# Kernel tuning notes

Measured on AMD Instinct MI355X. Metric: run time of the kernel, lower is better.

The kernel has to match this reference:

```python
import jax, jax.numpy as jnp
import numpy as np

N_NODES = 50000
N_EDGES = 800000
D = 96
H2 = 32
OUT = 4


def _glorot(key, shape):
    fan_in, fan_out = shape[0], shape[1]
    lim = (6.0 / (fan_in + fan_out)) ** 0.5
    return jax.random.uniform(key, shape, jnp.float32, -lim, lim)


def setup_inputs() -> dict:
    key = jax.random.key(0)
    ks = jax.random.split(key, 12)
    x = jax.random.normal(ks[0], (N_NODES, D), jnp.float32)
    edge_index = jax.random.randint(ks[1], (2, N_EDGES), 0, N_NODES, jnp.int32)
    return {
        "x": x,
        "edge_index": edge_index,
        "eps1": jnp.float32(0.0),
        "eps2": jnp.float32(0.0),
        "W1a": _glorot(ks[2], (D, D)),  "b1a": jnp.zeros((D,), jnp.float32),
        "W1b": _glorot(ks[3], (D, D)),  "b1b": jnp.zeros((D,), jnp.float32),
        "W2a": _glorot(ks[4], (D, H2)), "b2a": jnp.zeros((H2,), jnp.float32),
        "W2b": _glorot(ks[5], (H2, H2)),"b2b": jnp.zeros((H2,), jnp.float32),
        "Wh": _glorot(ks[6], (H2, OUT)),"bh": jnp.zeros((OUT,), jnp.float32),
    }


def _gin_agg(h, src, dst):
    # sum_{j in N(i)} h_j : gather source features, scatter-add to destination
    return jax.ops.segment_sum(h[src], dst, num_segments=N_NODES)


def reference(x, edge_index, eps1, eps2, W1a, b1a, W1b, b1b, W2a, b2a, W2b, b2b, Wh, bh):
    src, dst = edge_index[0], edge_index[1]

    # GIN layer 1: mlp1((1+eps1)*x + agg(x)), then outer ReLU (dropout is eval-mode identity)
    z = (1.0 + eps1) * x + _gin_agg(x, src, dst)           # [N, D]
    h = jax.nn.relu(z @ W1a + b1a) @ W1b + b1b             # mlp1
    h = jax.nn.relu(h)

    # GIN layer 2: mlp2((1+eps2)*h + agg(h)), then outer ReLU
    z2 = (1.0 + eps2) * h + _gin_agg(h, src, dst)          # [N, D]
    h2 = jax.nn.relu(z2 @ W2a + b2a) @ W2b + b2b           # mlp2 -> [N, 32]
    h2 = jax.nn.relu(h2)

    return h2 @ Wh + bh                                    # [N, 4]
```

## Files before the change

### kernel.cpp

```cpp
#include <hip/hip_runtime.h>

#define NN 50000
#define NE 800000
#define DD 96
#define HH 32
#define OO 4
#define ELLW 64
#define NBUCK 196
#define BCAP 8192

typedef unsigned short ushort_t;
typedef unsigned int uint_t;
typedef __attribute__((ext_vector_type(8))) short short8;
typedef __attribute__((ext_vector_type(4))) float f32x4;

__device__ inline ushort_t f2bf(float f) {
    uint_t b = __float_as_uint(f);
    return (ushort_t)((b + 0x7fffu + ((b >> 16) & 1u)) >> 16);
}

__device__ inline void addbf8(float* a, uint4 u) {
    a[0] += __uint_as_float(u.x << 16);
    a[1] += __uint_as_float(u.x & 0xffff0000u);
    a[2] += __uint_as_float(u.y << 16);
    a[3] += __uint_as_float(u.y & 0xffff0000u);
    a[4] += __uint_as_float(u.z << 16);
    a[5] += __uint_as_float(u.z & 0xffff0000u);
    a[6] += __uint_as_float(u.w << 16);
    a[7] += __uint_as_float(u.w & 0xffff0000u);
}


#define BA_B   98
#define WF_B   6
#define MT1    (NN / 16)
#define MFMA1_B ((MT1 + 3) / 4)

__global__ void k_big1(const int* __restrict__ edges, int* __restrict__ bcnt,
                       uint_t* __restrict__ packed,
                       const float* __restrict__ W1b, const float* __restrict__ W2a,
                       ushort_t* __restrict__ wf,
                       const float* __restrict__ x, const float* __restrict__ W1a,
                       ushort_t* __restrict__ y1) {
    int b = blockIdx.x;
    if (b < BA_B) {
        __shared__ int hist[NBUCK];
        __shared__ int basesh[NBUCK];
        int thr = threadIdx.x;
        if (thr < NBUCK) hist[thr] = 0;
        __syncthreads();
#pragma unroll
        for (int k = 0; k < 8; ++k) {
            int t4 = b * 2048 + k * 256 + thr;
            if (t4 < NE / 4) {
                int4 tt = ((const int4*)(edges + NE))[t4];
                atomicAdd(&hist[tt.x >> 8], 1);
                atomicAdd(&hist[tt.y >> 8], 1);
                atomicAdd(&hist[tt.z >> 8], 1);
                atomicAdd(&hist[tt.w >> 8], 1);
            }
        }
        __syncthreads();
        if (thr < NBUCK) {
            int c = hist[thr];
            basesh[thr] = c ? atomicAdd(&bcnt[thr], c) : 0;
        }
        __syncthreads();
        if (thr < NBUCK) hist[thr] = 0;
        __syncthreads();
#pragma unroll
        for (int k = 0; k < 8; ++k) {
            int t4 = b * 2048 + k * 256 + thr;
            if (t4 < NE / 4) {
                int4 ss = ((const int4*)edges)[t4];
                int4 tt = ((const int4*)(edges + NE))[t4];
                int b0 = tt.x >> 8, b1 = tt.y >> 8, b2 = tt.z >> 8, b3 = tt.w >> 8;
                int p0 = basesh[b0] + atomicAdd(&hist[b0], 1);
                int p1 = basesh[b1] + atomicAdd(&hist[b1], 1);
                int p2 = basesh[b2] + atomicAdd(&hist[b2], 1);
                int p3 = basesh[b3] + atomicAdd(&hist[b3], 1);
                if (p0 < BCAP) packed[(size_t)b0 * BCAP + p0] = ((uint_t)ss.x << 8) | (tt.x & 255);
                if (p1 < BCAP) packed[(size_t)b1 * BCAP + p1] = ((uint_t)ss.y << 8) | (tt.y & 255);
                if (p2 < BCAP) packed[(size_t)b2 * BCAP + p2] = ((uint_t)ss.z << 8) | (tt.z & 255);
                if (p3 < BCAP) packed[(size_t)b3 * BCAP + p3] = ((uint_t)ss.w << 8) | (tt.w & 255);
            }
        }
        return;
    }
    b -= BA_B;
    if (b < WF_B) {
        int tw = b * 256 + threadIdx.x;
        if (tw < 1152 + 384) {
            const float* Wsrc; ushort_t* dst; int KOUT, fl;
            if (tw < 1152) { Wsrc = W1b; dst = wf;        KOUT = DD; fl = tw; }
            else           { Wsrc = W2a; dst = wf + 9216; KOUT = HH; fl = tw - 1152; }
            int lane = fl & 63;
            int fc = fl >> 6;
            int c = fc % 3, nt = fc / 3;
            int kb = c * 32 + (lane >> 4) * 8;
            int col = nt * 16 + (lane & 15);
            ushort_t v[8];
#pragma unroll
            for (int j = 0; j < 8; ++j)
                v[j] = f2bf(Wsrc[(size_t)(kb + j) * KOUT + col]);
            *(uint4*)(dst + (size_t)fl * 8) = *(uint4*)v;
        }
        return;
    }
    b -= WF_B;
    constexpr int KC = 3, NT = 6;
    int lane = threadIdx.x & 63;
    int widx = threadIdx.x >> 6;
    int tile = b * 4 + widx;
    if (tile >= MT1) return;
    int row0 = tile * 16;
    int q = lane >> 4;
    int l16 = lane & 15;

    short8 bf[NT][KC];
#pragma unroll
    for (int nt = 0; nt < NT; ++nt)
#pragma unroll
        for (int c = 0; c < KC; ++c) {
            ushort_t v[8];
#pragma unroll
            for (int j = 0; j < 8; ++j)
                v[j] = f2bf(W1a[(size_t)(c * 32 + q * 8 + j) * DD + nt * 16 + l16]);
            bf[nt][c] = *(short8*)v;
        }

    short8 af[KC];
#pragma unroll
    for (int c = 0; c < KC; ++c) {
        const float* ap = x + (size_t)(row0 + l16) * DD + c * 32 + q * 8;
        float4 f0 = *(const float4*)ap;
        float4 f1 = *(const float4*)(ap + 4);
        ushort_t v[8] = {f2bf(f0.x), f2bf(f0.y), f2bf(f0.z), f2bf(f0.w),
                         f2bf(f1.x), f2bf(f1.y), f2bf(f1.z), f2bf(f1.w)};
        af[c] = *(short8*)v;
    }

    f32x4 acc[NT];
#pragma unroll
    for (int nt = 0; nt < NT; ++nt) acc[nt] = (f32x4){0.f, 0.f, 0.f, 0.f};
#pragma unroll
    for (int nt = 0; nt < NT; ++nt)
#pragma unroll
        for (int c = 0; c < KC; ++c)
            acc[nt] = __builtin_amdgcn_mfma_f32_16x16x32_bf16(af[c], bf[nt][c], acc[nt], 0, 0, 0);

#pragma unroll
    for (int nt = 0; nt < NT; ++nt) {
        int s = nt >> 1;
        int c32 = (nt & 1) * 16 + l16;
#pragma unroll
        for (int r = 0; r < 4; ++r)
            y1[(size_t)s * NN * 32 + (size_t)(row0 + q * 4 + r) * 32 + c32] = f2bf(acc[nt][r]);
    }
}


__global__ void k_bucketB(const int* __restrict__ bcnt, const uint_t* __restrict__ packed,
                          ushort_t* __restrict__ ell, int* __restrict__ deg) {
    __shared__ int curL[256];
    int b = blockIdx.x;
    int thr = threadIdx.x;
    int n0 = b * 256;
    curL[thr] = 0;
    __syncthreads();
    int cnt = min(bcnt[b], BCAP);
    const uint_t* pk = packed + (size_t)b * BCAP;
    for (int e = thr; e < cnt; e += 256) {
        uint_t u = pk[e];
        int doff = u & 255;
        int src = u >> 8;
        int p = atomicAdd(&curL[doff], 1);
        if (p < ELLW) ell[(size_t)(n0 + doff) * ELLW + p] = (ushort_t)src;
    }
    __syncthreads();
    if (n0 + thr < NN) deg[n0 + thr] = curL[thr];
}


__global__ void k_aggb96(const ushort_t* __restrict__ y, const int* __restrict__ deg,
                         const ushort_t* __restrict__ ell, const float* __restrict__ eps_p,
                         const float* __restrict__ b, ushort_t* __restrict__ out) {
    int idx = blockIdx.x * blockDim.x + threadIdx.x;
    if (idx >= NN * 24) return;
    int s = idx / (NN * 8);
    int rem = idx - s * (NN * 8);
    int i = rem >> 3;
    int sub = rem & 7;
    int v = sub >> 1, part = sub & 1;
    const uint4* ys = (const uint4*)(y + (size_t)s * NN * 32);
    const ushort_t* er = ell + (size_t)i * ELLW;
    int d = min(deg[i], ELLW);
    float a0[8] = {0,0,0,0,0,0,0,0}, a1[8] = {0,0,0,0,0,0,0,0};
    float a2[8] = {0,0,0,0,0,0,0,0}, a3[8] = {0,0,0,0,0,0,0,0};
    int p = part;
    for (; p + 6 < d; p += 8) {
        int s0 = er[p], s1 = er[p+2], s2 = er[p+4], s3 = er[p+6];
        uint4 f0 = ys[(size_t)s0 * 4 + v];
        uint4 f1 = ys[(size_t)s1 * 4 + v];
        uint4 f2 = ys[(size_t)s2 * 4 + v];
        uint4 f3 = ys[(size_t)s3 * 4 + v];
        addbf8(a0, f0); addbf8(a1, f1); addbf8(a2, f2); addbf8(a3, f3);
    }
    for (; p < d; p += 2) addbf8(a0, ys[(size_t)er[p] * 4 + v]);

    float sm[8];
#pragma unroll
    for (int k = 0; k < 8; ++k) {
        sm[k] = (a0[k] + a1[k]) + (a2[k] + a3[k]);
        sm[k] += __shfl_xor(sm[k], 1);
    }
    if (part) return;

    uint4 su = ys[(size_t)i * 4 + v];
    float s8[8];
    s8[0] = __uint_as_float(su.x << 16); s8[1] = __uint_as_float(su.x & 0xffff0000u);
    s8[2] = __uint_as_float(su.y << 16); s8[3] = __uint_as_float(su.y & 0xffff0000u);
    s8[4] = __uint_as_float(su.z << 16); s8[5] = __uint_as_float(su.z & 0xffff0000u);
    s8[6] = __uint_as_float(su.w << 16); s8[7] = __uint_as_float(su.w & 0xffff0000u);
    float4 bl = ((const float4*)b)[s * 8 + v * 2];
    float4 bhv = ((const float4*)b)[s * 8 + v * 2 + 1];
    float bb[8] = {bl.x, bl.y, bl.z, bl.w, bhv.x, bhv.y, bhv.z, bhv.w};
    float e = 1.0f + eps_p[0];
    ushort_t r[8];
#pragma unroll
    for (int k = 0; k < 8; ++k) {
        float vv = fmaf(e, s8[k], sm[k]) + bb[k];
        r[k] = f2bf(fmaxf(vv, 0.0f));
    }
    uint4 o;
    o.x = (uint_t)r[0] | ((uint_t)r[1] << 16);
    o.y = (uint_t)r[2] | ((uint_t)r[3] << 16);
    o.z = (uint_t)r[4] | ((uint_t)r[5] << 16);
    o.w = (uint_t)r[6] | ((uint_t)r[7] << 16);
    ((uint4*)out)[(size_t)i * 12 + s * 4 + v] = o;
}


#define HSTRIDE 104

__global__ void k_mfma23(const ushort_t* __restrict__ t1, const ushort_t* __restrict__ wf,
                         const float* __restrict__ b1b, ushort_t* __restrict__ y2) {
    constexpr int KC = 3, NT1 = 6, NT2 = 2;
    __shared__ __align__(16) ushort_t hT[4][16 * HSTRIDE];
    int lane = threadIdx.x & 63;
    int widx = threadIdx.x >> 6;
    int tile = blockIdx.x * 4 + widx;
    bool live = tile < MT1;
    int row0 = tile * 16;
    int q = lane >> 4;
    int l16 = lane & 15;
    const short8* bfp1 = (const short8*)wf;
    const short8* bfp2 = (const short8*)(wf + 9216);

    if (live) {
        short8 bf[NT1][KC];
#pragma unroll
        for (int nt = 0; nt < NT1; ++nt)
#pragma unroll
            for (int c = 0; c < KC; ++c)
                bf[nt][c] = bfp1[(nt * KC + c) * 64 + lane];

        short8 af[KC];
#pragma unroll
        for (int c = 0; c < KC; ++c) {
            uint4 av = *(const uint4*)(t1 + (size_t)(row0 + l16) * DD + c * 32 + q * 8);
            af[c] = *(short8*)&av;
        }

        f32x4 acc[NT1];
#pragma unroll
        for (int nt = 0; nt < NT1; ++nt) acc[nt] = (f32x4){0.f, 0.f, 0.f, 0.f};
#pragma unroll
        for (int nt = 0; nt < NT1; ++nt)
#pragma unroll
            for (int c = 0; c < KC; ++c)
                acc[nt] = __builtin_amdgcn_mfma_f32_16x16x32_bf16(af[c], bf[nt][c], acc[nt], 0, 0, 0);

#pragma unroll
        for (int nt = 0; nt < NT1; ++nt) {
            int col = nt * 16 + l16;
            float bv = b1b[col];
#pragma unroll
            for (int r = 0; r < 4; ++r)
                hT[widx][(q * 4 + r) * HSTRIDE + col] = f2bf(fmaxf(acc[nt][r] + bv, 0.0f));
        }
    }
    __syncthreads();
    if (!live) return;

    short8 af2[KC];
#pragma unroll
    for (int c = 0; c < KC; ++c) {
        uint4 av = *(const uint4*)&hT[widx][l16 * HSTRIDE + c * 32 + q * 8];
        af2[c] = *(short8*)&av;
    }
    short8 bf2[NT2][KC];
#pragma unroll
    for (int nt = 0; nt < NT2; ++nt)
#pragma unroll
        for (int c = 0; c < KC; ++c)
            bf2[nt][c] = bfp2[(nt * KC + c) * 64 + lane];

    f32x4 acc2[NT2];
#pragma unroll
    for (int nt = 0; nt < NT2; ++nt) acc2[nt] = (f32x4){0.f, 0.f, 0.f, 0.f};
#pragma unroll
    for (int nt = 0; nt < NT2; ++nt)
#pragma unroll
        for (int c = 0; c < KC; ++c)
            acc2[nt] = __builtin_amdgcn_mfma_f32_16x16x32_bf16(af2[c], bf2[nt][c], acc2[nt], 0, 0, 0);

#pragma unroll
    for (int nt = 0; nt < NT2; ++nt) {
        int col = nt * 16 + l16;
#pragma unroll
        for (int r = 0; r < 4; ++r)
            y2[(size_t)(row0 + q * 4 + r) * HH + col] = f2bf(acc2[nt][r]);
    }
}


#define TSTRIDE 36
#define ATR 16

__global__ void k_aggtail(const ushort_t* __restrict__ y2, const int* __restrict__ deg,
                          const ushort_t* __restrict__ ell, const float* __restrict__ eps_p,
                          const float* __restrict__ b2a, const float* __restrict__ W2b,
                          const float* __restrict__ b2b, const float* __restrict__ Wh,
                          const float* __restrict__ bhp, float* __restrict__ out) {
    __shared__ float t2f[ATR * TSTRIDE];
    int row = threadIdx.x >> 4;
    int sub = threadIdx.x & 15;
    int jg = sub & 3;
    int part = sub >> 2;
    int i = blockIdx.x * ATR + row;
    bool live = i < NN;

    if (live) {
        const uint4* y4 = (const uint4*)y2;
        const ushort_t* er = ell + (size_t)i * ELLW;
        int d = min(deg[i], ELLW);
        float a0[8] = {0,0,0,0,0,0,0,0}, a1[8] = {0,0,0,0,0,0,0,0};
        int p = part;
        for (; p + 4 < d; p += 8) {
            int s0 = er[p], s1 = er[p + 4];
            uint4 f0 = y4[(size_t)s0 * 4 + jg];
            uint4 f1 = y4[(size_t)s1 * 4 + jg];
            addbf8(a0, f0); addbf8(a1, f1);
        }
        for (; p < d; p += 4) addbf8(a0, y4[(size_t)er[p] * 4 + jg]);

        float s[8];
#pragma unroll
        for (int k = 0; k < 8; ++k) {
            s[k] = a0[k] + a1[k];
            s[k] += __shfl_xor(s[k], 4);
            s[k] += __shfl_xor(s[k], 8);
        }
        if (part == 0) {
            uint4 su = y4[(size_t)i * 4 + jg];
            float s8[8];
            s8[0] = __uint_as_float(su.x << 16); s8[1] = __uint_as_float(su.x & 0xffff0000u);
            s8[2] = __uint_as_float(su.y << 16); s8[3] = __uint_as_float(su.y & 0xffff0000u);
            s8[4] = __uint_as_float(su.z << 16); s8[5] = __uint_as_float(su.z & 0xffff0000u);
            s8[6] = __uint_as_float(su.w << 16); s8[7] = __uint_as_float(su.w & 0xffff0000u);
            float4 bl = ((const float4*)b2a)[2 * jg];
            float4 bhv = ((const float4*)b2a)[2 * jg + 1];
            float bb[8] = {bl.x, bl.y, bl.z, bl.w, bhv.x, bhv.y, bhv.z, bhv.w};
            float e = 1.0f + eps_p[0];
#pragma unroll
            for (int k = 0; k < 8; ++k) {
                float vv = fmaf(e, s8[k], s[k]) + bb[k];
                t2f[row * TSTRIDE + jg * 8 + k] = fmaxf(vv, 0.0f);
            }
        }
    }
    __syncthreads();

    float o[OO] = {0.f, 0.f, 0.f, 0.f};
    if (live) {
        const float* tr = &t2f[row * TSTRIDE];
#pragma unroll
        for (int jj = 0; jj < 2; ++jj) {
            int j = sub * 2 + jj;
            float acc = b2b[j];
#pragma unroll 8
            for (int k = 0; k < HH; ++k)
                acc = fmaf(tr[k], W2b[k * HH + j], acc);
            acc = fmaxf(acc, 0.0f);
#pragma unroll
            for (int oo = 0; oo < OO; ++oo)
                o[oo] = fmaf(acc, Wh[j * OO + oo], o[oo]);
        }
    }
#pragma unroll
    for (int oo = 0; oo < OO; ++oo) {
        o[oo] += __shfl_xor(o[oo], 1);
        o[oo] += __shfl_xor(o[oo], 2);
        o[oo] += __shfl_xor(o[oo], 4);
        o[oo] += __shfl_xor(o[oo], 8);
    }
    if (live && sub == 0) {
        float4 ov = {o[0] + bhp[0], o[1] + bhp[1], o[2] + bhp[2], o[3] + bhp[3]};
        ((float4*)out)[i] = ov;
    }
}


extern "C" void kernel_launch(void* const* d_in, const int* in_sizes, int n_in,
                              void* d_out, int out_size, void* d_ws, size_t ws_size,
                              hipStream_t stream) {
    const float* x    = (const float*)d_in[0];
    const int*   edges= (const int*)d_in[1];
    const float* eps1 = (const float*)d_in[2];
    const float* eps2 = (const float*)d_in[3];
    const float* W1a  = (const float*)d_in[4];
    const float* b1a  = (const float*)d_in[5];
    const float* W1b  = (const float*)d_in[6];
    const float* b1b  = (const float*)d_in[7];
    const float* W2a  = (const float*)d_in[8];
    const float* b2a  = (const float*)d_in[9];
    const float* W2b  = (const float*)d_in[10];
    const float* b2b  = (const float*)d_in[11];
    const float* Wh   = (const float*)d_in[12];
    const float* bh   = (const float*)d_in[13];

    auto al = [](size_t n) { return (n + 255) / 256 * 256; };
    char* w = (char*)d_ws;
    int*      bcnt   = (int*)w;      w += al((size_t)NBUCK * 4);
    uint_t*   packed = (uint_t*)w;   w += al((size_t)NBUCK * BCAP * 4);
    int*      deg    = (int*)w;      w += al((size_t)NN * 4);
    ushort_t* ell    = (ushort_t*)w; w += al((size_t)NN * ELLW * 2);
    ushort_t* wf     = (ushort_t*)w; w += al((size_t)(9216 + 3072) * 2);
    ushort_t* y1     = (ushort_t*)w; w += al((size_t)NN * DD * 2);
    ushort_t* t1     = (ushort_t*)w; w += al((size_t)NN * DD * 2);
    ushort_t* y2     = (ushort_t*)w; w += al((size_t)NN * HH * 2);

    const int B = 256;

    hipMemsetAsync(bcnt, 0, (size_t)NBUCK * 4, stream);
    k_big1<<<BA_B + WF_B + MFMA1_B, B, 0, stream>>>(edges, bcnt, packed, W1b, W2a, wf,
                                                    x, W1a, y1);
    k_bucketB<<<NBUCK, B, 0, stream>>>(bcnt, packed, ell, deg);
    k_aggb96<<<(NN * 24 + B - 1) / B, B, 0, stream>>>(y1, deg, ell, eps1, b1a, t1);
    k_mfma23<<<MFMA1_B, B, 0, stream>>>(t1, wf, b1b, y2);
    k_aggtail<<<(NN + ATR - 1) / ATR, B, 0, stream>>>(y2, deg, ell, eps2, b2a, W2b, b2b,
                                                      Wh, bh, (float*)d_out);
}
```

Baseline: 187.9 us.

## Rebalance fused kernels: move layer-1 MFMA alongside bucket fill, stage W1a in LDS

The edge-partitioning pass now runs alone in a smaller pre-kernel with twice as many blocks and half the work per block. The layer-1 x@W1a MFMA moves into the bucket-fill kernel so it overlaps with ELL construction. Each MFMA block converts W1a to bf16 fragments once into LDS instead of every wave converting from global memory. The cost is an extra per-block LDS staging pass plus a barrier, and the dense GEMM no longer overlaps with the histogram pass.

New measurement: 182.3 us (median of 2 runs). 3.0% less time.

```diff
diff --git a/kernel.cpp b/kernel.cpp
--- a/kernel.cpp
+++ b/kernel.cpp
@@ -31,17 +31,13 @@
 }
 
 
-#define BA_B   98
+#define BA_B   196
 #define WF_B   6
-#define MT1    (NN / 16)
-#define MFMA1_B ((MT1 + 3) / 4)
-
-__global__ void k_big1(const int* __restrict__ edges, int* __restrict__ bcnt,
-                       uint_t* __restrict__ packed,
-                       const float* __restrict__ W1b, const float* __restrict__ W2a,
-                       ushort_t* __restrict__ wf,
-                       const float* __restrict__ x, const float* __restrict__ W1a,
-                       ushort_t* __restrict__ y1) {
+
+__global__ void k_pre(const int* __restrict__ edges, int* __restrict__ bcnt,
+                      uint_t* __restrict__ packed,
+                      const float* __restrict__ W1b, const float* __restrict__ W2a,
+                      ushort_t* __restrict__ wf) {
     int b = blockIdx.x;
     if (b < BA_B) {
         __shared__ int hist[NBUCK];
@@ -50,8 +46,8 @@
         if (thr < NBUCK) hist[thr] = 0;
         __syncthreads();
 #pragma unroll
-        for (int k = 0; k < 8; ++k) {
-            int t4 = b * 2048 + k * 256 + thr;
+        for (int k = 0; k < 4; ++k) {
+            int t4 = b * 1024 + k * 256 + thr;
             if (t4 < NE / 4) {
                 int4 tt = ((const int4*)(edges + NE))[t4];
                 atomicAdd(&hist[tt.x >> 8], 1);
@@ -69,8 +65,8 @@
         if (thr < NBUCK) hist[thr] = 0;
         __syncthreads();
 #pragma unroll
-        for (int k = 0; k < 8; ++k) {
-            int t4 = b * 2048 + k * 256 + thr;
+        for (int k = 0; k < 4; ++k) {
+            int t4 = b * 1024 + k * 256 + thr;
             if (t4 < NE / 4) {
                 int4 ss = ((const int4*)edges)[t4];
                 int4 tt = ((const int4*)(edges + NE))[t4];
@@ -88,29 +84,71 @@
         return;
     }
     b -= BA_B;
-    if (b < WF_B) {
-        int tw = b * 256 + threadIdx.x;
-        if (tw < 1152 + 384) {
-            const float* Wsrc; ushort_t* dst; int KOUT, fl;
-            if (tw < 1152) { Wsrc = W1b; dst = wf;        KOUT = DD; fl = tw; }
-            else           { Wsrc = W2a; dst = wf + 9216; KOUT = HH; fl = tw - 1152; }
-            int lane = fl & 63;
-            int fc = fl >> 6;
-            int c = fc % 3, nt = fc / 3;
-            int kb = c * 32 + (lane >> 4) * 8;
-            int col = nt * 16 + (lane & 15);
-            ushort_t v[8];
-#pragma unroll
-            for (int j = 0; j < 8; ++j)
-                v[j] = f2bf(Wsrc[(size_t)(kb + j) * KOUT + col]);
-            *(uint4*)(dst + (size_t)fl * 8) = *(uint4*)v;
-        }
+    int tw = b * 256 + threadIdx.x;
+    if (tw < 1152 + 384) {
+        const float* Wsrc; ushort_t* dst; int KOUT, fl;
+        if (tw < 1152) { Wsrc = W1b; dst = wf;        KOUT = DD; fl = tw; }
+        else           { Wsrc = W2a; dst = wf + 9216; KOUT = HH; fl = tw - 1152; }
+        int lane = fl & 63;
+        int fc = fl >> 6;
+        int c = fc % 3, nt = fc / 3;
+        int kb = c * 32 + (lane >> 4) * 8;
+        int col = nt * 16 + (lane & 15);
+        ushort_t v[8];
+#pragma unroll
+        for (int j = 0; j < 8; ++j)
+            v[j] = f2bf(Wsrc[(size_t)(kb + j) * KOUT + col]);
+        *(uint4*)(dst + (size_t)fl * 8) = *(uint4*)v;
+    }
+}
+
+
+#define MT1    (NN / 16)
+#define MFMA1_B ((MT1 + 3) / 4)
+
+__global__ void k_main(const int* __restrict__ bcnt, const uint_t* __restrict__ packed,
+                       ushort_t* __restrict__ ell, int* __restrict__ deg,
+                       const float* __restrict__ x, const float* __restrict__ W1a,
+                       ushort_t* __restrict__ y1) {
+    __shared__ __align__(16) ushort_t lds[1152 * 8];
+    int b = blockIdx.x;
+    int thr = threadIdx.x;
+    if (b < NBUCK) {
+        int* curL = (int*)lds;
+        int n0 = b * 256;
+        curL[thr] = 0;
+        __syncthreads();
+        int cnt = min(bcnt[b], BCAP);
+        const uint_t* pk = packed + (size_t)b * BCAP;
+        for (int e = thr; e < cnt; e += 256) {
+            uint_t u = pk[e];
+            int doff = u & 255;
+            int src = u >> 8;
+            int p = atomicAdd(&curL[doff], 1);
+            if (p < ELLW) ell[(size_t)(n0 + doff) * ELLW + p] = (ushort_t)src;
+        }
+        __syncthreads();
+        if (n0 + thr < NN) deg[n0 + thr] = curL[thr];
         return;
     }
-    b -= WF_B;
+    b -= NBUCK;
     constexpr int KC = 3, NT = 6;
-    int lane = threadIdx.x & 63;
-    int widx = threadIdx.x >> 6;
+    for (int fl = thr; fl < 1152; fl += 256) {
+        int lane_f = fl & 63;
+        int fc = fl >> 6;
+        int c = fc % 3, nt = fc / 3;
+        int kb = c * 32 + (lane_f >> 4) * 8;
+        int col = nt * 16 + (lane_f & 15);
+        ushort_t v[8];
+#pragma unroll
+        for (int j = 0; j < 8; ++j)
+            v[j] = f2bf(W1a[(size_t)(kb + j) * DD + col]);
+        *(uint4*)(lds + (size_t)fl * 8) = *(uint4*)v;
+    }
+    __syncthreads();
+
+    int lane = thr & 63;
+    int widx = thr >> 6;
     int tile = b * 4 + widx;
     if (tile >= MT1) return;
     int row0 = tile * 16;
@@ -121,13 +159,8 @@
 #pragma unroll
     for (int nt = 0; nt < NT; ++nt)
 #pragma unroll
-        for (int c = 0; c < KC; ++c) {
-            ushort_t v[8];
-#pragma unroll
-            for (int j = 0; j < 8; ++j)
-                v[j] = f2bf(W1a[(size_t)(c * 32 + q * 8 + j) * DD + nt * 16 + l16]);
-            bf[nt][c] = *(short8*)v;
-        }
+        for (int c = 0; c < KC; ++c)
+            bf[nt][c] = *(short8*)(lds + ((size_t)(nt * 3 + c) * 64 + lane) * 8);
 
     short8 af[KC];
 #pragma unroll
@@ -157,28 +190,6 @@
         for (int r = 0; r < 4; ++r)
             y1[(size_t)s * NN * 32 + (size_t)(row0 + q * 4 + r) * 32 + c32] = f2bf(acc[nt][r]);
     }
-}
-
-
-__global__ void k_bucketB(const int* __restrict__ bcnt, const uint_t* __restrict__ packed,
-                          ushort_t* __restrict__ ell, int* __restrict__ deg) {
-    __shared__ int curL[256];
-    int b = blockIdx.x;
-    int thr = threadIdx.x;
-    int n0 = b * 256;
-    curL[thr] = 0;
-    __syncthreads();
-    int cnt = min(bcnt[b], BCAP);
-    const uint_t* pk = packed + (size_t)b * BCAP;
-    for (int e = thr; e < cnt; e += 256) {
-        uint_t u = pk[e];
-        int doff = u & 255;
-        int src = u >> 8;
-        int p = atomicAdd(&curL[doff], 1);
-        if (p < ELLW) ell[(size_t)(n0 + doff) * ELLW + p] = (ushort_t)src;
-    }
-    __syncthreads();
-    if (n0 + thr < NN) deg[n0 + thr] = curL[thr];
 }
 
 
@@ -444,9 +455,8 @@
     const int B = 256;
 
     hipMemsetAsync(bcnt, 0, (size_t)NBUCK * 4, stream);
-    k_big1<<<BA_B + WF_B + MFMA1_B, B, 0, stream>>>(edges, bcnt, packed, W1b, W2a, wf,
-                                                    x, W1a, y1);
-    k_bucketB<<<NBUCK, B, 0, stream>>>(bcnt, packed, ell, deg);
+    k_pre<<<BA_B + WF_B, B, 0, stream>>>(edges, bcnt, packed, W1b, W2a, wf);
+    k_main<<<NBUCK + MFMA1_B, B, 0, stream>>>(bcnt, packed, ell, deg, x, W1a, y1);
     k_aggb96<<<(NN * 24 + B - 1) / B, B, 0, stream>>>(y1, deg, ell, eps1, b1a, t1);
     k_mfma23<<<MFMA1_B, B, 0, stream>>>(t1, wf, b1b, y2);
     k_aggtail<<<(NN + ATR - 1) / ATR, B, 0, stream>>>(y2, deg, ell, eps2, b2a, W2b, b2b,
```
